# Kernel tuning notes

Measured on AMD Instinct MI355X. Metric: run time of the kernel, lower is better.

## Reference

```python
import jax, jax.numpy as jnp
import numpy as np

# SS2D (VMamba) dims
B, H, W, C = 2, 48, 48, 96
D_INNER, D_STATE, DT_RANK, K = 192, 32, 6, 4


def _silu(x):
    return x * jax.nn.sigmoid(x)


def setup_inputs() -> dict:
    key = jax.random.key(0)
    ks = jax.random.split(key, 8)
    inputs = jax.random.normal(ks[0], (B, H, W, C), jnp.float32)
    in_proj_w = jax.random.normal(ks[1], (2 * D_INNER, C), jnp.float32) * 0.02
    conv_w = jax.random.normal(ks[2], (D_INNER, 1, 3, 3), jnp.float32) * 0.1
    conv_b = jnp.zeros((D_INNER,), jnp.float32)
    x_proj_w = jax.random.normal(ks[3], (K, DT_RANK + 2 * D_STATE, D_INNER), jnp.float32) * 0.02
    dt_projs_w = jax.random.normal(ks[4], (K, D_INNER, DT_RANK), jnp.float32) * 0.1
    dt_projs_b = jax.random.uniform(ks[5], (K, D_INNER), jnp.float32, -4.0, -2.0)
    # S4D-real init: A_log[n] = log(n+1), tiled over K*d_inner
    A_logs = jnp.log(jnp.tile(jnp.arange(1, D_STATE + 1, dtype=jnp.float32), (K * D_INNER, 1)))
    Ds = jnp.ones((K * D_INNER,), jnp.float32)
    ln_w = jnp.ones((D_INNER,), jnp.float32)
    ln_b = jnp.zeros((D_INNER,), jnp.float32)
    out_proj_w = jax.random.normal(ks[6], (C, D_INNER), jnp.float32) * 0.02
    return dict(inputs=inputs, in_proj_w=in_proj_w, conv_w=conv_w, conv_b=conv_b,
                x_proj_w=x_proj_w, dt_projs_w=dt_projs_w, dt_projs_b=dt_projs_b,
                A_logs=A_logs, Ds=Ds, ln_w=ln_w, ln_b=ln_b, out_proj_w=out_proj_w)


def _selective_scan(us, deltas, A, Bs, Cs, Ds_kd):
    # us, deltas: (B,K,d,L); Bs, Cs: (B,K,N,L); A: (K,d,N); Ds_kd: (K,d)
    u_l = jnp.moveaxis(us, -1, 0)      # (L,B,K,d)
    d_l = jnp.moveaxis(deltas, -1, 0)  # (L,B,K,d)
    B_l = jnp.moveaxis(Bs, -1, 0)      # (L,B,K,N)
    C_l = jnp.moveaxis(Cs, -1, 0)      # (L,B,K,N)
    h0 = jnp.zeros(us.shape[:3] + (A.shape[-1],), us.dtype)  # (B,K,d,N)

    def step(h, inp):
        u, d, b, c = inp
        dA = jnp.exp(d[..., None] * A)                    # (B,K,d,N)
        h = h * dA + (d * u)[..., None] * b[:, :, None, :]
        y = jnp.einsum('bkdn,bkn->bkd', h, c)
        return h, y

    _, ys = jax.lax.scan(step, h0, (u_l, d_l, B_l, C_l))
    ys = jnp.moveaxis(ys, 0, -1)  # (B,K,d,L)
    return ys + Ds_kd[None, :, :, None] * us


def _ss2d(x, in_proj_w, conv_w, conv_b, x_proj_w, dt_projs_w, dt_projs_b,
          A_logs, Ds, ln_w, ln_b, out_proj_w):
    b, h, w, c = x.shape
    L = h * w
    xz = jnp.einsum('bhwc,ec->bhwe', x, in_proj_w)          # (B,H,W,2*d_inner)
    x_, z = jnp.split(xz, 2, axis=-1)
    # depthwise 3x3 conv (NCHW), SAME padding
    x_ = jnp.transpose(x_, (0, 3, 1, 2))                    # (B,d,H,W)
    x_ = jax.lax.conv_general_dilated(x_, conv_w, (1, 1), 'SAME',
                                      feature_group_count=D_INNER,
                                      dimension_numbers=('NCHW', 'OIHW', 'NCHW'))
    x_ = _silu(x_ + conv_b[None, :, None, None])
    # 4-direction scan inputs
    x_hw = x_.reshape(b, D_INNER, L)
    x_wh = jnp.transpose(x_, (0, 1, 3, 2)).reshape(b, D_INNER, L)
    xs = jnp.stack([x_hw, x_wh], axis=1)                    # (B,2,d,L)
    xs = jnp.concatenate([xs, jnp.flip(xs, axis=-1)], axis=1)  # (B,4,d,L)
    x_dbl = jnp.einsum('bkdl,kcd->bkcl', xs, x_proj_w)      # (B,4,dt_rank+2N,L)
    dts = x_dbl[:, :, :DT_RANK]
    Bs = x_dbl[:, :, DT_RANK:DT_RANK + D_STATE]
    Cs = x_dbl[:, :, DT_RANK + D_STATE:]
    dts = jnp.einsum('bkrl,kdr->bkdl', dts, dt_projs_w)
    deltas = jax.nn.softplus(dts + dt_projs_b[None, :, :, None])
    A = -jnp.exp(A_logs).reshape(K, D_INNER, D_STATE)
    Ds_kd = Ds.reshape(K, D_INNER)
    out_y = _selective_scan(xs, deltas, A, Bs, Cs, Ds_kd)   # (B,4,d,L)
    inv_y = jnp.flip(out_y[:, 2:4], axis=-1)                # (B,2,d,L)
    wh_y = jnp.transpose(out_y[:, 1].reshape(b, D_INNER, w, h), (0, 1, 3, 2)).reshape(b, D_INNER, L)
    invwh_y = jnp.transpose(inv_y[:, 1].reshape(b, D_INNER, w, h), (0, 1, 3, 2)).reshape(b, D_INNER, L)
    y = out_y[:, 0] + inv_y[:, 0] + wh_y + invwh_y          # (B,d,L)
    y = jnp.transpose(y, (0, 2, 1)).reshape(b, h, w, D_INNER)
    # LayerNorm over channel dim
    mu = jnp.mean(y, axis=-1, keepdims=True)
    var = jnp.var(y, axis=-1, keepdims=True)
    y = (y - mu) * jax.lax.rsqrt(var + 1e-5) * ln_w + ln_b
    y = y * _silu(z)
    return jnp.einsum('bhwd,cd->bhwc', y, out_proj_w)


def reference(inputs, in_proj_w, conv_w, conv_b, x_proj_w, dt_projs_w, dt_projs_b,
              A_logs, Ds, ln_w, ln_b, out_proj_w):
    attn = _ss2d(inputs, in_proj_w, conv_w, conv_b, x_proj_w, dt_projs_w,
                 dt_projs_b, A_logs, Ds, ln_w, ln_b, out_proj_w)
    return inputs + attn
```

## Files before the change

### kernel.cpp

```cpp
#include <hip/hip_runtime.h>
#include <math.h>

#define B_ 2
#define H_ 48
#define W_ 48
#define C_ 96
#define D_ 192
#define L_ 2304
#define K_ 4
#define NS 32
#define RK 6
#define CD 70

#define NC 16
#define CL (L_/NC)
#define NCH (B_*K_*D_)

#define BDL (B_*D_*L_)
#define OFF_Z      0
#define OFF_XPRE   (OFF_Z    + BDL)
#define OFF_XHW    (OFF_XPRE + BDL)
#define OFF_XWH    (OFF_XHW  + BDL)
#define OFF_DELTA  (OFF_XWH  + BDL)
#define OFF_BS     (OFF_DELTA+ B_*K_*D_*L_)
#define OFF_CS     (OFF_BS   + B_*K_*L_*NS)
#define OFF_YS     (OFF_CS   + B_*K_*L_*NS)
#define OFF_YF     (OFF_YS   + B_*K_*L_*D_)

#define OFF_H0     OFF_YF

__global__ __launch_bounds__(256) void k1_inproj(const float* __restrict__ x,
        const float* __restrict__ w, float* __restrict__ ws) {
    __shared__ __align__(16) float Xs[24*128];
    int blk = blockIdx.x;
    int b = blk / 288;
    int rem = blk % 288;
    int l0 = (rem >> 2) * 32;
    int es = rem & 3;
    int tid = threadIdx.x;
    const float4* xs4 = (const float4*)(x + (size_t)(b*L_ + l0)*C_);
    #pragma unroll
    for (int it = 0; it < 3; ++it) {
        int i4 = it*256 + tid;
        float4 v = xs4[i4];
        int idx4 = i4*4;
        int p = idx4 / 96, c = idx4 % 96;
        *(float4*)&Xs[(c>>2)*128 + p*4] = v;
    }
    __syncthreads();
    int l = tid & 31, eg = tid >> 5;
    int pos = l0 + l;
    float acc[12];
    #pragma unroll
    for (int i = 0; i < 12; ++i) acc[i] = 0.f;
    const float4* wp[12];
    #pragma unroll
    for (int i = 0; i < 12; ++i) {
        int e = es*96 + eg*12 + i;
        wp[i] = (const float4*)(w + (size_t)e*96);
    }
    for (int q = 0; q < 24; ++q) {
        float4 xr = *(const float4*)&Xs[q*128 + l*4];
        #pragma unroll
        for (int i = 0; i < 12; ++i) {
            float4 wv = wp[i][q];
            acc[i] += xr.x*wv.x + xr.y*wv.y + xr.z*wv.z + xr.w*wv.w;
        }
    }
    if (es < 2) {
        float* xpre = ws + OFF_XPRE;
        #pragma unroll
        for (int i = 0; i < 12; ++i) {
            int e = es*96 + eg*12 + i;
            xpre[(size_t)(b*D_ + e)*L_ + pos] = acc[i];
        }
    } else {
        float* zp = ws + OFF_Z + (size_t)(b*L_ + pos)*D_ + (es-2)*96 + eg*12;
        #pragma unroll
        for (int q = 0; q < 3; ++q)
            *(float4*)&zp[q*4] = make_float4(acc[q*4], acc[q*4+1], acc[q*4+2], acc[q*4+3]);
    }
}

__global__ __launch_bounds__(256) void k2_conv(const float* __restrict__ cw,
        const float* __restrict__ cb, float* __restrict__ ws) {
    __shared__ float img[26*48];
    __shared__ float res[24*49];
    int blk = blockIdx.x;
    int bd = blk >> 1;
    int half = blk & 1;
    int d = bd % D_;
    int hh0 = half * 24;
    int tid = threadIdx.x;
    const float* xp = ws + OFF_XPRE + (size_t)bd*L_;
    for (int it = 0; it < 5; ++it) {
        int idx = it*256 + tid;
        if (idx < 26*48) {
            int gr = hh0 - 1 + idx/48;
            img[idx] = (gr >= 0 && gr < H_) ? xp[gr*48 + idx%48] : 0.f;
        }
    }
    float wr[9];
    #pragma unroll
    for (int j = 0; j < 9; ++j) wr[j] = cw[d*9 + j];
    float bias = cb[d];
    __syncthreads();
    float* hw = ws + OFF_XHW + (size_t)bd*L_ + hh0*48;
    for (int it = 0; it < 5; ++it) {
        int idx = it*256 + tid;
        if (idx < 24*48) {
            int r = idx/48, w0 = idx%48;
            float acc = bias;
            #pragma unroll
            for (int kh = 0; kh < 3; ++kh) {
                #pragma unroll
                for (int kw = 0; kw < 3; ++kw) {
                    int iw = w0 + kw - 1;
                    if (iw >= 0 && iw < W_)
                        acc = fmaf(img[(r+kh)*48 + iw], wr[kh*3 + kw], acc);
                }
            }
            float v = acc / (1.f + __expf(-acc));
            hw[idx] = v;
            res[r*49 + w0] = v;
        }
    }
    __syncthreads();
    float* wh = ws + OFF_XWH + (size_t)bd*L_;
    for (int it = 0; it < 5; ++it) {
        int idx = it*256 + tid;
        if (idx < 24*48) {
            int w0 = idx/24, r = idx%24;
            wh[w0*48 + hh0 + r] = res[r*49 + w0];
        }
    }
}

__global__ __launch_bounds__(256) void k3_xproj(const float* __restrict__ xpw,
        const float* __restrict__ dtw, const float* __restrict__ dtb,
        float* __restrict__ ws) {
    __shared__ __align__(16) float Xs[48*64];
    __shared__ float xd[CD*17];
    int blk = blockIdx.x;
    int b = blk / 576;
    int rem = blk % 576;
    int k = rem / 144;
    int l0 = (rem % 144) * 16;
    int tid = threadIdx.x;
    const float* src = ws + ((k & 1) ? OFF_XWH : OFF_XHW);
    bool flip = (k >= 2);
    #pragma unroll
    for (int it = 0; it < 12; ++it) {
        int idx = it*256 + tid;
        int d = idx >> 4, l = idx & 15;
        int pos = flip ? (L_ - 1 - (l0 + l)) : (l0 + l);
        Xs[(d>>2)*64 + l*4 + (d&3)] = src[(size_t)(b*D_ + d)*L_ + pos];
    }
    __syncthreads();
    int l = tid & 15, cg = tid >> 4;
    {
        float acc[5] = {0.f, 0.f, 0.f, 0.f, 0.f};
        const float4* wp[5];
        #pragma unroll
        for (int i = 0; i < 5; ++i) {
            int c = cg + 16*i;
            if (c >= CD) c = 0;
            wp[i] = (const float4*)(xpw + ((size_t)k*CD + c)*D_);
        }
        for (int q = 0; q < 48; ++q) {
            float4 xr = *(const float4*)&Xs[q*64 + l*4];
            #pragma unroll
            for (int i = 0; i < 5; ++i) {
                float4 wv = wp[i][q];
                acc[i] += xr.x*wv.x + xr.y*wv.y + xr.z*wv.z + xr.w*wv.w;
            }
        }
        #pragma unroll
        for (int i = 0; i < 5; ++i) {
            int c = cg + 16*i;
            if (c < CD) xd[c*17 + l] = acc[i];
        }
    }
    __syncthreads();
    {
        float r[6];
        #pragma unroll
        for (int rr = 0; rr < 6; ++rr) r[rr] = xd[rr*17 + l];
        float* dout = ws + OFF_DELTA + (size_t)(b*K_ + k)*D_*L_;
        int dg = tid >> 4;
        for (int i = 0; i < 12; ++i) {
            int d = dg*12 + i;
            const float* wdt = dtw + ((size_t)k*D_ + d)*6;
            float acc = dtb[k*D_ + d];
            #pragma unroll
            for (int rr = 0; rr < 6; ++rr) acc = fmaf(r[rr], wdt[rr], acc);
            float sp = fmaxf(acc, 0.f) + log1pf(__expf(-fabsf(acc)));
            dout[(size_t)d*L_ + l0 + l] = sp;
        }
    }
    {
        float* Bsp = ws + OFF_BS + ((size_t)(b*K_ + k)*L_ + l0)*NS;
        float* Csp = ws + OFF_CS + ((size_t)(b*K_ + k)*L_ + l0)*NS;
        int n = tid & 31, lq = tid >> 5;
        #pragma unroll
        for (int j = 0; j < 2; ++j) {
            int ll = lq + 8*j;
            Bsp[(size_t)ll*NS + n] = xd[(RK + n)*17 + ll];
            Csp[(size_t)ll*NS + n] = xd[(RK + NS + n)*17 + ll];
        }
    }
}

__global__ __launch_bounds__(512) void k4a_local(const float* __restrict__ Alogs,
        float* __restrict__ ws) {
    __shared__ float Pl[2][NC][NS];
    __shared__ float Hl[2][NC][NS];
    int blk = blockIdx.x;
    int bk = blk / 96;
    int p = blk % 96;
    int b = bk >> 2, k = bk & 3;
    int c = threadIdx.x >> 5;
    int n = threadIdx.x & 31;
    int dA = 2*p;
    float aA = -__expf(Alogs[((size_t)k*D_ + dA)*NS + n]);
    float aB = -__expf(Alogs[((size_t)k*D_ + dA + 1)*NS + n]);
    const float* dpA = ws + OFF_DELTA + (size_t)(bk*D_ + dA)*L_ + c*CL;
    const float* dpB = dpA + L_;
    const float* uA = ws + ((k & 1) ? OFF_XWH : OFF_XHW) + (size_t)(b*D_ + dA)*L_;
    const float* uB = uA + L_;
    const float* Bsp = ws + OFF_BS + ((size_t)bk*L_ + c*CL)*NS;
    bool flip = (k >= 2);
    float hA = 0.f, hB = 0.f, PA = 1.f, PB = 1.f;
    #pragma unroll 4
    for (int l = 0; l < CL; ++l) {
        int gl = c*CL + l;
        int gu = flip ? (L_ - 1 - gl) : gl;
        float dlA = dpA[l], dlB = dpB[l];
        float uAv = uA[gu], uBv = uB[gu];
        float bn = Bsp[l*NS + n];
        float eA = __expf(dlA * aA);
        float eB = __expf(dlB * aB);
        hA = fmaf(hA, eA, dlA*uAv*bn);
        hB = fmaf(hB, eB, dlB*uBv*bn);
        PA *= eA;
        PB *= eB;
    }
    Pl[0][c][n] = PA; Pl[1][c][n] = PB;
    Hl[0][c][n] = hA; Hl[1][c][n] = hB;
    __syncthreads();
    if (threadIdx.x < 64) {
        int ch = threadIdx.x >> 5, nn = threadIdx.x & 31;
        float* H0p = ws + OFF_H0 + (size_t)(bk*D_ + dA + ch)*NC*NS + nn;
        float h = 0.f;
        #pragma unroll
        for (int cc = 0; cc < NC; ++cc) {
            H0p[cc*NS] = h;
            h = fmaf(h, Pl[ch][cc][nn], Hl[ch][cc][nn]);
        }
    }
}

__global__ __launch_bounds__(512) void k4c_scan(const float* __restrict__ Alogs,
        const float* __restrict__ Dsp, float* __restrict__ ws) {
    __shared__ float yld[CL*32];
    int blk = blockIdx.x;
    int dg = blk % 6;
    int c  = (blk / 6) % NC;
    int bk = blk / (6*NC);
    int b = bk >> 2, k = bk & 3;
    int sw = threadIdx.x >> 5;
    int n  = threadIdx.x & 31;
    int dA = dg*32 + sw;
    int dB = dA + 16;
    float aA = -__expf(Alogs[((size_t)k*D_ + dA)*NS + n]);
    float aB = -__expf(Alogs[((size_t)k*D_ + dB)*NS + n]);
    float dcA = Dsp[k*D_ + dA];
    float dcB = Dsp[k*D_ + dB];
    const float* dpA = ws + OFF_DELTA + (size_t)(bk*D_ + dA)*L_ + c*CL;
    const float* dpB = dpA + 16*L_;
    const float* uA = ws + ((k & 1) ? OFF_XWH : OFF_XHW) + (size_t)(b*D_ + dA)*L_;
    const float* uB = uA + 16*L_;
    const float* Bsp = ws + OFF_BS + ((size_t)bk*L_ + c*CL)*NS;
    const float* Csp = ws + OFF_CS + ((size_t)bk*L_ + c*CL)*NS;
    bool flip = (k >= 2);
    float hA = ws[OFF_H0 + (size_t)(bk*D_ + dA)*NC*NS + c*NS + n];
    float hB = ws[OFF_H0 + (size_t)(bk*D_ + dB)*NC*NS + c*NS + n];
    int g = n >> 3;
    int off = ((g & 1) << 1) | (g >> 1);
    for (int lb = 0; lb < CL; lb += 4) {
        float yA[4], yB[4], uuA[4], uuB[4];
        #pragma unroll
        for (int j = 0; j < 4; ++j) {
            int l = lb + j;
            int gl = c*CL + l;
            int gu = flip ? (L_ - 1 - gl) : gl;
            float dlA = dpA[l], dlB = dpB[l];
            float uAv = uA[gu], uBv = uB[gu];
            float bn = Bsp[l*NS + n];
            float cn = Csp[l*NS + n];
            hA = fmaf(hA, __expf(dlA*aA), dlA*uAv*bn);
            hB = fmaf(hB, __expf(dlB*aB), dlB*uBv*bn);
            yA[j] = hA * cn; yB[j] = hB * cn;
            uuA[j] = uAv;    uuB[j] = uBv;
        }
        #pragma unroll
        for (int j = 0; j < 4; ++j) {
            yA[j] += __shfl_xor(yA[j], 16);
            yB[j] += __shfl_xor(yB[j], 16);
        }
        float zA0 = (n & 16) ? yA[1] : yA[0];
        float zA1 = (n & 16) ? yA[3] : yA[2];
        float zB0 = (n & 16) ? yB[1] : yB[0];
        float zB1 = (n & 16) ? yB[3] : yB[2];
        zA0 += __shfl_xor(zA0, 8); zA1 += __shfl_xor(zA1, 8);
        zB0 += __shfl_xor(zB0, 8); zB1 += __shfl_xor(zB1, 8);
        float wA = (n & 8) ? zA1 : zA0;
        float wB = (n & 8) ? zB1 : zB0;
        wA += __shfl_xor(wA, 4); wA += __shfl_xor(wA, 2); wA += __shfl_xor(wA, 1);
        wB += __shfl_xor(wB, 4); wB += __shfl_xor(wB, 2); wB += __shfl_xor(wB, 1);
        float uaA = (n & 16) ? uuA[1] : uuA[0];
        float ubA = (n & 16) ? uuA[3] : uuA[2];
        float usA = (n & 8) ? ubA : uaA;
        float uaB = (n & 16) ? uuB[1] : uuB[0];
        float ubB = (n & 16) ? uuB[3] : uuB[2];
        float usB = (n & 8) ? ubB : uaB;
        if ((n & 7) == 0) {
            yld[(lb + off)*32 + sw]      = fmaf(dcA, usA, wA);
            yld[(lb + off)*32 + sw + 16] = fmaf(dcB, usB, wB);
        }
    }
    __syncthreads();
    float* ysp = ws + OFF_YS + ((size_t)bk*L_ + c*CL)*D_ + dg*32;
    #pragma unroll
    for (int it = 0; it < 9; ++it) {
        int idx = it*512 + threadIdx.x;
        int l = idx >> 5, dd = idx & 31;
        ysp[(size_t)l*D_ + dd] = yld[idx];
    }
}

__global__ __launch_bounds__(192) void k5_combine(const float* __restrict__ lnw,
        const float* __restrict__ lnb, float* __restrict__ ws) {
    int bp = blockIdx.x;
    int b = bp / L_, pos = bp % L_;
    int d = threadIdx.x;
    int hh = pos / W_, w0 = pos % W_;
    int poswh = w0*H_ + hh;
    const float* ys = ws + OFF_YS + (size_t)b*K_*L_*D_;
    float y = ys[(size_t)(0*L_ + pos)*D_ + d]
            + ys[(size_t)(2*L_ + (L_ - 1 - pos))*D_ + d]
            + ys[(size_t)(1*L_ + poswh)*D_ + d]
            + ys[(size_t)(3*L_ + (L_ - 1 - poswh))*D_ + d];
    float s = y, ss = y*y;
    #pragma unroll
    for (int m = 32; m >= 1; m >>= 1) {
        s  += __shfl_xor(s, m);
        ss += __shfl_xor(ss, m);
    }
    __shared__ float red[2][4];
    int wv = threadIdx.x >> 6;
    if ((threadIdx.x & 63) == 0) { red[0][wv] = s; red[1][wv] = ss; }
    __syncthreads();
    float su = red[0][0] + red[0][1] + red[0][2];
    float sq = red[1][0] + red[1][1] + red[1][2];
    float mu  = su * (1.f/192.f);
    float var = sq * (1.f/192.f) - mu*mu;
    float rs  = rsqrtf(var + 1e-5f);
    float yn = (y - mu)*rs*lnw[d] + lnb[d];
    float zv = ws[OFF_Z + (size_t)(b*L_ + pos)*D_ + d];
    float sz = zv / (1.f + __expf(-zv));
    ws[OFF_YF + (size_t)(b*L_ + pos)*D_ + d] = yn * sz;
}

__global__ __launch_bounds__(256) void k6_outproj(const float* __restrict__ w,
        const float* __restrict__ xin, float* __restrict__ out,
        const float* __restrict__ ws) {
    __shared__ __align__(16) float Ys[48*64];
    __shared__ float outT[16*49];
    int blk = blockIdx.x;
    int b = blk / 288;
    int rem = blk % 288;
    int l0 = (rem >> 1) * 16;
    int es = rem & 1;
    int tid = threadIdx.x;
    const float4* yf4 = (const float4*)(ws + OFF_YF + (size_t)(b*L_ + l0)*D_);
    #pragma unroll
    for (int it = 0; it < 3; ++it) {
        int i4 = it*256 + tid;
        float4 v = yf4[i4];
        int idx4 = i4*4;
        int p = idx4 / 192, dd = idx4 % 192;
        *(float4*)&Ys[(dd>>2)*64 + p*4] = v;
    }
    __syncthreads();
    int l = tid & 15, cg = tid >> 4;
    float acc[3] = {0.f, 0.f, 0.f};
    const float4* wp[3];
    #pragma unroll
    for (int i = 0; i < 3; ++i) {
        int c = es*48 + cg*3 + i;
        wp[i] = (const float4*)(w + (size_t)c*D_);
    }
    for (int q = 0; q < 48; ++q) {
        float4 xr = *(const float4*)&Ys[q*64 + l*4];
        #pragma unroll
        for (int i = 0; i < 3; ++i) {
            float4 wv = wp[i][q];
            acc[i] += xr.x*wv.x + xr.y*wv.y + xr.z*wv.z + xr.w*wv.w;
        }
    }
    #pragma unroll
    for (int i = 0; i < 3; ++i) outT[l*49 + cg*3 + i] = acc[i];
    __syncthreads();
    #pragma unroll
    for (int it = 0; it < 3; ++it) {
        int idx = it*256 + tid;
        int p = idx / 48, cc = idx % 48;
        size_t o = (size_t)(b*L_ + l0 + p)*C_ + es*48 + cc;
        out[o] = xin[o] + outT[p*49 + cc];
    }
}

extern "C" void kernel_launch(void* const* d_in, const int* in_sizes, int n_in,
                              void* d_out, int out_size, void* d_ws, size_t ws_size,
                              hipStream_t stream) {
    const float* x        = (const float*)d_in[0];
    const float* in_proj  = (const float*)d_in[1];
    const float* conv_w   = (const float*)d_in[2];
    const float* conv_b   = (const float*)d_in[3];
    const float* x_proj_w = (const float*)d_in[4];
    const float* dt_w     = (const float*)d_in[5];
    const float* dt_b     = (const float*)d_in[6];
    const float* A_logs   = (const float*)d_in[7];
    const float* Ds       = (const float*)d_in[8];
    const float* ln_w     = (const float*)d_in[9];
    const float* ln_b     = (const float*)d_in[10];
    const float* out_w    = (const float*)d_in[11];
    float* out = (float*)d_out;
    float* ws  = (float*)d_ws;

    k1_inproj <<<576,  256, 0, stream>>>(x, in_proj, ws);
    k2_conv   <<<768,  256, 0, stream>>>(conv_w, conv_b, ws);
    k3_xproj  <<<1152, 256, 0, stream>>>(x_proj_w, dt_w, dt_b, ws);
    k4a_local <<<768,  512, 0, stream>>>(A_logs, ws);
    k4c_scan  <<<768,  512, 0, stream>>>(A_logs, Ds, ws);
    k5_combine<<<B_*L_,192, 0, stream>>>(ln_w, ln_b, ws);
    k6_outproj<<<576,  256, 0, stream>>>(out_w, x, out, ws);
}
```

Before: 284.2 us.

## Transpose B/C layout, vectorize scan loads, use exp2, fuse LayerNorm with out-projection

Stores B and C as (N, L) instead of (L, N) so the scan kernels can read them with float4 loads along L. The chunk-local and chunk scans now load delta, u, B and C as float4, use a native exp2 with prescaled A, and derive the chunk decay product from the sum of deltas. The chunk scan processes 8 steps per iteration, folds the D*u skip term into the reduction, and pads its shared buffer to cut bank conflicts. The combine+LayerNorm+gate kernel is fused with the out-projection, which removes the YF round trip through global memory and one launch. The trade-off is fewer blocks in the fused kernel (288) and higher register pressure in the scan.

Measured after the change: 340.3 us. 19.8% more time.

```diff
diff --git a/kernel.cpp b/kernel.cpp
--- a/kernel.cpp
+++ b/kernel.cpp
@@ -15,6 +15,15 @@
 #define NC 16
 #define CL (L_/NC)
 #define NCH (B_*K_*D_)
+#define LOG2E 1.44269504088896f
+
+__device__ __forceinline__ float fexp2(float x) {
+#if __has_builtin(__builtin_amdgcn_exp2f)
+    return __builtin_amdgcn_exp2f(x);
+#else
+    return __expf(x * 0.69314718055994531f);
+#endif
+}
 
 #define BDL (B_*D_*L_)
 #define OFF_Z      0
@@ -199,14 +208,14 @@
         }
     }
     {
-        float* Bsp = ws + OFF_BS + ((size_t)(b*K_ + k)*L_ + l0)*NS;
-        float* Csp = ws + OFF_CS + ((size_t)(b*K_ + k)*L_ + l0)*NS;
-        int n = tid & 31, lq = tid >> 5;
+        float* Bb = ws + OFF_BS + (size_t)(b*K_ + k)*NS*L_;
+        float* Cb = ws + OFF_CS + (size_t)(b*K_ + k)*NS*L_;
+        int ll = tid & 15, nh = tid >> 4;
         #pragma unroll
         for (int j = 0; j < 2; ++j) {
-            int ll = lq + 8*j;
-            Bsp[(size_t)ll*NS + n] = xd[(RK + n)*17 + ll];
-            Csp[(size_t)ll*NS + n] = xd[(RK + NS + n)*17 + ll];
+            int n = nh + 16*j;
+            Bb[(size_t)n*L_ + l0 + ll] = xd[(RK + n)*17 + ll];
+            Cb[(size_t)n*L_ + l0 + ll] = xd[(RK + NS + n)*17 + ll];
         }
     }
 }
@@ -222,47 +231,67 @@
     int c = threadIdx.x >> 5;
     int n = threadIdx.x & 31;
     int dA = 2*p;
-    float aA = -__expf(Alogs[((size_t)k*D_ + dA)*NS + n]);
-    float aB = -__expf(Alogs[((size_t)k*D_ + dA + 1)*NS + n]);
+    float a2A = -__expf(Alogs[((size_t)k*D_ + dA)*NS + n]) * LOG2E;
+    float a2B = -__expf(Alogs[((size_t)k*D_ + dA + 1)*NS + n]) * LOG2E;
     const float* dpA = ws + OFF_DELTA + (size_t)(bk*D_ + dA)*L_ + c*CL;
     const float* dpB = dpA + L_;
-    const float* uA = ws + ((k & 1) ? OFF_XWH : OFF_XHW) + (size_t)(b*D_ + dA)*L_;
-    const float* uB = uA + L_;
-    const float* Bsp = ws + OFF_BS + ((size_t)bk*L_ + c*CL)*NS;
+    const float* uAp = ws + ((k & 1) ? OFF_XWH : OFF_XHW) + (size_t)(b*D_ + dA)*L_;
+    const float* uBp = uAp + L_;
+    const float* Bp = ws + OFF_BS + ((size_t)bk*NS + n)*L_ + c*CL;
     bool flip = (k >= 2);
-    float hA = 0.f, hB = 0.f, PA = 1.f, PB = 1.f;
-    #pragma unroll 4
-    for (int l = 0; l < CL; ++l) {
-        int gl = c*CL + l;
-        int gu = flip ? (L_ - 1 - gl) : gl;
-        float dlA = dpA[l], dlB = dpB[l];
-        float uAv = uA[gu], uBv = uB[gu];
-        float bn = Bsp[l*NS + n];
-        float eA = __expf(dlA * aA);
-        float eB = __expf(dlB * aB);
-        hA = fmaf(hA, eA, dlA*uAv*bn);
-        hB = fmaf(hB, eB, dlB*uBv*bn);
-        PA *= eA;
-        PB *= eB;
-    }
-    Pl[0][c][n] = PA; Pl[1][c][n] = PB;
+    float hA = 0.f, hB = 0.f, sdA = 0.f, sdB = 0.f;
+    for (int lb = 0; lb < CL; lb += 4) {
+        float4 dA4 = *(const float4*)(dpA + lb);
+        float4 dB4 = *(const float4*)(dpB + lb);
+        float4 b4  = *(const float4*)(Bp + lb);
+        float4 tA4, tB4;
+        if (!flip) {
+            tA4 = *(const float4*)(uAp + c*CL + lb);
+            tB4 = *(const float4*)(uBp + c*CL + lb);
+        } else {
+            float4 rA = *(const float4*)(uAp + (L_ - 4) - (c*CL + lb));
+            float4 rB = *(const float4*)(uBp + (L_ - 4) - (c*CL + lb));
+            tA4 = make_float4(rA.w, rA.z, rA.y, rA.x);
+            tB4 = make_float4(rB.w, rB.z, rB.y, rB.x);
+        }
+        float dlA[4] = {dA4.x, dA4.y, dA4.z, dA4.w};
+        float dlB[4] = {dB4.x, dB4.y, dB4.z, dB4.w};
+        float uuA[4] = {tA4.x, tA4.y, tA4.z, tA4.w};
+        float uuB[4] = {tB4.x, tB4.y, tB4.z, tB4.w};
+        float bb[4]  = {b4.x, b4.y, b4.z, b4.w};
+        #pragma unroll
+        for (int j = 0; j < 4; ++j) {
+            float eA = fexp2(dlA[j]*a2A);
+            float eB = fexp2(dlB[j]*a2B);
+            hA = fmaf(hA, eA, dlA[j]*uuA[j]*bb[j]);
+            hB = fmaf(hB, eB, dlB[j]*uuB[j]*bb[j]);
+            sdA += dlA[j]; sdB += dlB[j];
+        }
+    }
+    Pl[0][c][n] = fexp2(a2A*sdA);
+    Pl[1][c][n] = fexp2(a2B*sdB);
     Hl[0][c][n] = hA; Hl[1][c][n] = hB;
     __syncthreads();
     if (threadIdx.x < 64) {
         int ch = threadIdx.x >> 5, nn = threadIdx.x & 31;
-        float* H0p = ws + OFF_H0 + (size_t)(bk*D_ + dA + ch)*NC*NS + nn;
-        float h = 0.f;
+        float hh = 0.f;
         #pragma unroll
         for (int cc = 0; cc < NC; ++cc) {
-            H0p[cc*NS] = h;
-            h = fmaf(h, Pl[ch][cc][nn], Hl[ch][cc][nn]);
-        }
-    }
+            float pr = Pl[ch][cc][nn];
+            float hf = Hl[ch][cc][nn];
+            Pl[ch][cc][nn] = hh;
+            hh = fmaf(hh, pr, hf);
+        }
+    }
+    __syncthreads();
+    #pragma unroll
+    for (int ch = 0; ch < 2; ++ch)
+        ws[OFF_H0 + (size_t)(bk*D_ + dA + ch)*NC*NS + c*NS + n] = Pl[ch][c][n];
 }
 
 __global__ __launch_bounds__(512) void k4c_scan(const float* __restrict__ Alogs,
         const float* __restrict__ Dsp, float* __restrict__ ws) {
-    __shared__ float yld[CL*32];
+    __shared__ float yld[CL*33];
     int blk = blockIdx.x;
     int dg = blk % 6;
     int c  = (blk / 6) % NC;
@@ -272,61 +301,99 @@
     int n  = threadIdx.x & 31;
     int dA = dg*32 + sw;
     int dB = dA + 16;
-    float aA = -__expf(Alogs[((size_t)k*D_ + dA)*NS + n]);
-    float aB = -__expf(Alogs[((size_t)k*D_ + dB)*NS + n]);
-    float dcA = Dsp[k*D_ + dA];
-    float dcB = Dsp[k*D_ + dB];
+    float a2A = -__expf(Alogs[((size_t)k*D_ + dA)*NS + n]) * LOG2E;
+    float a2B = -__expf(Alogs[((size_t)k*D_ + dB)*NS + n]) * LOG2E;
+    float dc32A = Dsp[k*D_ + dA] * (1.f/32.f);
+    float dc32B = Dsp[k*D_ + dB] * (1.f/32.f);
     const float* dpA = ws + OFF_DELTA + (size_t)(bk*D_ + dA)*L_ + c*CL;
     const float* dpB = dpA + 16*L_;
-    const float* uA = ws + ((k & 1) ? OFF_XWH : OFF_XHW) + (size_t)(b*D_ + dA)*L_;
-    const float* uB = uA + 16*L_;
-    const float* Bsp = ws + OFF_BS + ((size_t)bk*L_ + c*CL)*NS;
-    const float* Csp = ws + OFF_CS + ((size_t)bk*L_ + c*CL)*NS;
+    const float* uAp = ws + ((k & 1) ? OFF_XWH : OFF_XHW) + (size_t)(b*D_ + dA)*L_;
+    const float* uBp = uAp + 16*L_;
+    const float* Bp = ws + OFF_BS + ((size_t)bk*NS + n)*L_ + c*CL;
+    const float* Cp = ws + OFF_CS + ((size_t)bk*NS + n)*L_ + c*CL;
     bool flip = (k >= 2);
     float hA = ws[OFF_H0 + (size_t)(bk*D_ + dA)*NC*NS + c*NS + n];
     float hB = ws[OFF_H0 + (size_t)(bk*D_ + dB)*NC*NS + c*NS + n];
-    int g = n >> 3;
-    int off = ((g & 1) << 1) | (g >> 1);
-    for (int lb = 0; lb < CL; lb += 4) {
-        float yA[4], yB[4], uuA[4], uuB[4];
-        #pragma unroll
-        for (int j = 0; j < 4; ++j) {
-            int l = lb + j;
-            int gl = c*CL + l;
-            int gu = flip ? (L_ - 1 - gl) : gl;
-            float dlA = dpA[l], dlB = dpB[l];
-            float uAv = uA[gu], uBv = uB[gu];
-            float bn = Bsp[l*NS + n];
-            float cn = Csp[l*NS + n];
-            hA = fmaf(hA, __expf(dlA*aA), dlA*uAv*bn);
-            hB = fmaf(hB, __expf(dlB*aB), dlB*uBv*bn);
-            yA[j] = hA * cn; yB[j] = hB * cn;
-            uuA[j] = uAv;    uuB[j] = uBv;
-        }
-        #pragma unroll
-        for (int j = 0; j < 4; ++j) {
+    int off = ((n>>4)&1)*4 + ((n>>3)&1)*2 + ((n>>2)&1);
+    for (int lb = 0; lb < CL; lb += 8) {
+        float dlA[8], dlB[8], uuA[8], uuB[8], bb[8], cc8[8];
+        {
+            float4 a0 = *(const float4*)(dpA + lb);
+            float4 a1 = *(const float4*)(dpA + lb + 4);
+            float4 b0 = *(const float4*)(dpB + lb);
+            float4 b1 = *(const float4*)(dpB + lb + 4);
+            dlA[0]=a0.x; dlA[1]=a0.y; dlA[2]=a0.z; dlA[3]=a0.w;
+            dlA[4]=a1.x; dlA[5]=a1.y; dlA[6]=a1.z; dlA[7]=a1.w;
+            dlB[0]=b0.x; dlB[1]=b0.y; dlB[2]=b0.z; dlB[3]=b0.w;
+            dlB[4]=b1.x; dlB[5]=b1.y; dlB[6]=b1.z; dlB[7]=b1.w;
+            float4 v0 = *(const float4*)(Bp + lb);
+            float4 v1 = *(const float4*)(Bp + lb + 4);
+            bb[0]=v0.x; bb[1]=v0.y; bb[2]=v0.z; bb[3]=v0.w;
+            bb[4]=v1.x; bb[5]=v1.y; bb[6]=v1.z; bb[7]=v1.w;
+            float4 c0 = *(const float4*)(Cp + lb);
+            float4 c1 = *(const float4*)(Cp + lb + 4);
+            cc8[0]=c0.x; cc8[1]=c0.y; cc8[2]=c0.z; cc8[3]=c0.w;
+            cc8[4]=c1.x; cc8[5]=c1.y; cc8[6]=c1.z; cc8[7]=c1.w;
+            if (!flip) {
+                float4 u0 = *(const float4*)(uAp + c*CL + lb);
+                float4 u1 = *(const float4*)(uAp + c*CL + lb + 4);
+                float4 w0 = *(const float4*)(uBp + c*CL + lb);
+                float4 w1 = *(const float4*)(uBp + c*CL + lb + 4);
+                uuA[0]=u0.x; uuA[1]=u0.y; uuA[2]=u0.z; uuA[3]=u0.w;
+                uuA[4]=u1.x; uuA[5]=u1.y; uuA[6]=u1.z; uuA[7]=u1.w;
+                uuB[0]=w0.x; uuB[1]=w0.y; uuB[2]=w0.z; uuB[3]=w0.w;
+                uuB[4]=w1.x; uuB[5]=w1.y; uuB[6]=w1.z; uuB[7]=w1.w;
+            } else {
+                float4 u0 = *(const float4*)(uAp + (L_ - 4) - (c*CL + lb));
+                float4 u1 = *(const float4*)(uAp + (L_ - 8) - (c*CL + lb));
+                float4 w0 = *(const float4*)(uBp + (L_ - 4) - (c*CL + lb));
+                float4 w1 = *(const float4*)(uBp + (L_ - 8) - (c*CL + lb));
+                uuA[0]=u0.w; uuA[1]=u0.z; uuA[2]=u0.y; uuA[3]=u0.x;
+                uuA[4]=u1.w; uuA[5]=u1.z; uuA[6]=u1.y; uuA[7]=u1.x;
+                uuB[0]=w0.w; uuB[1]=w0.z; uuB[2]=w0.y; uuB[3]=w0.x;
+                uuB[4]=w1.w; uuB[5]=w1.z; uuB[6]=w1.y; uuB[7]=w1.x;
+            }
+        }
+        float yA[8], yB[8];
+        #pragma unroll
+        for (int j = 0; j < 8; ++j) {
+            float eA = fexp2(dlA[j]*a2A);
+            float eB = fexp2(dlB[j]*a2B);
+            hA = fmaf(hA, eA, dlA[j]*uuA[j]*bb[j]);
+            hB = fmaf(hB, eB, dlB[j]*uuB[j]*bb[j]);
+            yA[j] = fmaf(hA, cc8[j], dc32A*uuA[j]);
+            yB[j] = fmaf(hB, cc8[j], dc32B*uuB[j]);
+        }
+        #pragma unroll
+        for (int j = 0; j < 8; ++j) {
             yA[j] += __shfl_xor(yA[j], 16);
             yB[j] += __shfl_xor(yB[j], 16);
         }
-        float zA0 = (n & 16) ? yA[1] : yA[0];
-        float zA1 = (n & 16) ? yA[3] : yA[2];
-        float zB0 = (n & 16) ? yB[1] : yB[0];
-        float zB1 = (n & 16) ? yB[3] : yB[2];
+        float zA0 = (n & 16) ? yA[4] : yA[0];
+        float zA1 = (n & 16) ? yA[5] : yA[1];
+        float zA2 = (n & 16) ? yA[6] : yA[2];
+        float zA3 = (n & 16) ? yA[7] : yA[3];
+        float zB0 = (n & 16) ? yB[4] : yB[0];
+        float zB1 = (n & 16) ? yB[5] : yB[1];
+        float zB2 = (n & 16) ? yB[6] : yB[2];
+        float zB3 = (n & 16) ? yB[7] : yB[3];
         zA0 += __shfl_xor(zA0, 8); zA1 += __shfl_xor(zA1, 8);
+        zA2 += __shfl_xor(zA2, 8); zA3 += __shfl_xor(zA3, 8);
         zB0 += __shfl_xor(zB0, 8); zB1 += __shfl_xor(zB1, 8);
-        float wA = (n & 8) ? zA1 : zA0;
-        float wB = (n & 8) ? zB1 : zB0;
-        wA += __shfl_xor(wA, 4); wA += __shfl_xor(wA, 2); wA += __shfl_xor(wA, 1);
-        wB += __shfl_xor(wB, 4); wB += __shfl_xor(wB, 2); wB += __shfl_xor(wB, 1);
-        float uaA = (n & 16) ? uuA[1] : uuA[0];
-        float ubA = (n & 16) ? uuA[3] : uuA[2];
-        float usA = (n & 8) ? ubA : uaA;
-        float uaB = (n & 16) ? uuB[1] : uuB[0];
-        float ubB = (n & 16) ? uuB[3] : uuB[2];
-        float usB = (n & 8) ? ubB : uaB;
-        if ((n & 7) == 0) {
-            yld[(lb + off)*32 + sw]      = fmaf(dcA, usA, wA);
-            yld[(lb + off)*32 + sw + 16] = fmaf(dcB, usB, wB);
+        zB2 += __shfl_xor(zB2, 8); zB3 += __shfl_xor(zB3, 8);
+        float wA0 = (n & 8) ? zA2 : zA0;
+        float wA1 = (n & 8) ? zA3 : zA1;
+        float wB0 = (n & 8) ? zB2 : zB0;
+        float wB1 = (n & 8) ? zB3 : zB1;
+        wA0 += __shfl_xor(wA0, 4); wA1 += __shfl_xor(wA1, 4);
+        wB0 += __shfl_xor(wB0, 4); wB1 += __shfl_xor(wB1, 4);
+        float tA = (n & 4) ? wA1 : wA0;
+        float tB = (n & 4) ? wB1 : wB0;
+        tA += __shfl_xor(tA, 2); tA += __shfl_xor(tA, 1);
+        tB += __shfl_xor(tB, 2); tB += __shfl_xor(tB, 1);
+        if ((n & 3) == 0) {
+            yld[(lb + off)*33 + sw]      = tA;
+            yld[(lb + off)*33 + sw + 16] = tB;
         }
     }
     __syncthreads();
@@ -335,89 +402,98 @@
     for (int it = 0; it < 9; ++it) {
         int idx = it*512 + threadIdx.x;
         int l = idx >> 5, dd = idx & 31;
-        ysp[(size_t)l*D_ + dd] = yld[idx];
-    }
-}
-
-__global__ __launch_bounds__(192) void k5_combine(const float* __restrict__ lnw,
-        const float* __restrict__ lnb, float* __restrict__ ws) {
-    int bp = blockIdx.x;
-    int b = bp / L_, pos = bp % L_;
-    int d = threadIdx.x;
-    int hh = pos / W_, w0 = pos % W_;
-    int poswh = w0*H_ + hh;
-    const float* ys = ws + OFF_YS + (size_t)b*K_*L_*D_;
-    float y = ys[(size_t)(0*L_ + pos)*D_ + d]
-            + ys[(size_t)(2*L_ + (L_ - 1 - pos))*D_ + d]
-            + ys[(size_t)(1*L_ + poswh)*D_ + d]
-            + ys[(size_t)(3*L_ + (L_ - 1 - poswh))*D_ + d];
-    float s = y, ss = y*y;
-    #pragma unroll
-    for (int m = 32; m >= 1; m >>= 1) {
-        s  += __shfl_xor(s, m);
-        ss += __shfl_xor(ss, m);
-    }
-    __shared__ float red[2][4];
-    int wv = threadIdx.x >> 6;
-    if ((threadIdx.x & 63) == 0) { red[0][wv] = s; red[1][wv] = ss; }
-    __syncthreads();
-    float su = red[0][0] + red[0][1] + red[0][2];
-    float sq = red[1][0] + red[1][1] + red[1][2];
-    float mu  = su * (1.f/192.f);
-    float var = sq * (1.f/192.f) - mu*mu;
-    float rs  = rsqrtf(var + 1e-5f);
-    float yn = (y - mu)*rs*lnw[d] + lnb[d];
-    float zv = ws[OFF_Z + (size_t)(b*L_ + pos)*D_ + d];
-    float sz = zv / (1.f + __expf(-zv));
-    ws[OFF_YF + (size_t)(b*L_ + pos)*D_ + d] = yn * sz;
-}
-
-__global__ __launch_bounds__(256) void k6_outproj(const float* __restrict__ w,
+        ysp[(size_t)l*D_ + dd] = yld[l*33 + dd];
+    }
+}
+
+__global__ __launch_bounds__(256) void k56_fused(const float* __restrict__ lnw,
+        const float* __restrict__ lnb, const float* __restrict__ w,
         const float* __restrict__ xin, float* __restrict__ out,
         const float* __restrict__ ws) {
-    __shared__ __align__(16) float Ys[48*64];
-    __shared__ float outT[16*49];
+    __shared__ __align__(16) float YsT[16*196];
+    __shared__ float psum[16][17], psq[16][17];
+    __shared__ float outT[16*97];
     int blk = blockIdx.x;
-    int b = blk / 288;
-    int rem = blk % 288;
-    int l0 = (rem >> 1) * 16;
-    int es = rem & 1;
+    int b = blk / 144;
+    int l0 = (blk % 144) * 16;
     int tid = threadIdx.x;
-    const float4* yf4 = (const float4*)(ws + OFF_YF + (size_t)(b*L_ + l0)*D_);
-    #pragma unroll
-    for (int it = 0; it < 3; ++it) {
-        int i4 = it*256 + tid;
-        float4 v = yf4[i4];
-        int idx4 = i4*4;
-        int p = idx4 / 192, dd = idx4 % 192;
-        *(float4*)&Ys[(dd>>2)*64 + p*4] = v;
-    }
-    __syncthreads();
-    int l = tid & 15, cg = tid >> 4;
-    float acc[3] = {0.f, 0.f, 0.f};
-    const float4* wp[3];
-    #pragma unroll
-    for (int i = 0; i < 3; ++i) {
-        int c = es*48 + cg*3 + i;
-        wp[i] = (const float4*)(w + (size_t)c*D_);
-    }
-    for (int q = 0; q < 48; ++q) {
-        float4 xr = *(const float4*)&Ys[q*64 + l*4];
-        #pragma unroll
-        for (int i = 0; i < 3; ++i) {
-            float4 wv = wp[i][q];
-            acc[i] += xr.x*wv.x + xr.y*wv.y + xr.z*wv.z + xr.w*wv.w;
-        }
-    }
-    #pragma unroll
-    for (int i = 0; i < 3; ++i) outT[l*49 + cg*3 + i] = acc[i];
-    __syncthreads();
-    #pragma unroll
-    for (int it = 0; it < 3; ++it) {
+    {
+        int p = tid >> 4, dg = tid & 15;
+        int pos = l0 + p;
+        int hh = pos / W_, w0 = pos % W_;
+        int poswh = w0*H_ + hh;
+        const float* ysb = ws + OFF_YS + (size_t)b*K_*L_*D_;
+        const float* r0 = ysb + (size_t)(0*L_ + pos)*D_;
+        const float* r1 = ysb + (size_t)(1*L_ + poswh)*D_;
+        const float* r2 = ysb + (size_t)(2*L_ + (L_-1-pos))*D_;
+        const float* r3 = ysb + (size_t)(3*L_ + (L_-1-poswh))*D_;
+        float yv[12];
+        float s = 0.f, sq = 0.f;
+        #pragma unroll
+        for (int i = 0; i < 12; i += 4) {
+            int d = dg*12 + i;
+            float4 v0 = *(const float4*)(r0 + d);
+            float4 v1 = *(const float4*)(r1 + d);
+            float4 v2 = *(const float4*)(r2 + d);
+            float4 v3 = *(const float4*)(r3 + d);
+            float y0 = v0.x+v1.x+v2.x+v3.x;
+            float y1 = v0.y+v1.y+v2.y+v3.y;
+            float y2 = v0.z+v1.z+v2.z+v3.z;
+            float y3 = v0.w+v1.w+v2.w+v3.w;
+            yv[i]=y0; yv[i+1]=y1; yv[i+2]=y2; yv[i+3]=y3;
+            s += y0+y1+y2+y3;
+            sq += y0*y0+y1*y1+y2*y2+y3*y3;
+        }
+        psum[p][dg] = s; psq[p][dg] = sq;
+        __syncthreads();
+        float su = 0.f, ssq = 0.f;
+        #pragma unroll
+        for (int j = 0; j < 16; ++j) { su += psum[p][j]; ssq += psq[p][j]; }
+        float mu  = su * (1.f/192.f);
+        float var = ssq * (1.f/192.f) - mu*mu;
+        float rs  = rsqrtf(var + 1e-5f);
+        const float* zp = ws + OFF_Z + (size_t)(b*L_ + pos)*D_;
+        #pragma unroll
+        for (int i = 0; i < 12; i += 4) {
+            int d = dg*12 + i;
+            float4 o;
+            float* oo = (float*)&o;
+            #pragma unroll
+            for (int jj = 0; jj < 4; ++jj) {
+                float yn = (yv[i+jj] - mu)*rs*lnw[d+jj] + lnb[d+jj];
+                float zv = zp[d+jj];
+                float sz = zv / (1.f + __expf(-zv));
+                oo[jj] = yn * sz;
+            }
+            *(float4*)&YsT[p*196 + d] = o;
+        }
+    }
+    __syncthreads();
+    {
+        int l = tid & 15, cg = tid >> 4;
+        float acc[6] = {0.f,0.f,0.f,0.f,0.f,0.f};
+        const float4* wp[6];
+        #pragma unroll
+        for (int i = 0; i < 6; ++i)
+            wp[i] = (const float4*)(w + (size_t)(cg*6 + i)*D_);
+        for (int q = 0; q < 48; ++q) {
+            float4 xr = *(const float4*)&YsT[l*196 + q*4];
+            #pragma unroll
+            for (int i = 0; i < 6; ++i) {
+                float4 wv = wp[i][q];
+                acc[i] += xr.x*wv.x + xr.y*wv.y + xr.z*wv.z + xr.w*wv.w;
+            }
+        }
+        #pragma unroll
+        for (int i = 0; i < 6; ++i) outT[l*97 + cg*6 + i] = acc[i];
+    }
+    __syncthreads();
+    #pragma unroll
+    for (int it = 0; it < 6; ++it) {
         int idx = it*256 + tid;
-        int p = idx / 48, cc = idx % 48;
-        size_t o = (size_t)(b*L_ + l0 + p)*C_ + es*48 + cc;
-        out[o] = xin[o] + outT[p*49 + cc];
+        int p = idx / 96, cc = idx % 96;
+        size_t o = (size_t)(b*L_ + l0 + p)*C_ + cc;
+        out[o] = xin[o] + outT[p*97 + cc];
     }
 }
 
@@ -444,6 +520,5 @@
     k3_xproj  <<<1152, 256, 0, stream>>>(x_proj_w, dt_w, dt_b, ws);
     k4a_local <<<768,  512, 0, stream>>>(A_logs, ws);
     k4c_scan  <<<768,  512, 0, stream>>>(A_logs, Ds, ws);
-    k5_combine<<<B_*L_,192, 0, stream>>>(ln_w, ln_b, ws);
-    k6_outproj<<<576,  256, 0, stream>>>(out_w, x, out, ws);
-}
+    k56_fused <<<288,  256, 0, stream>>>(ln_w, ln_b, out_w, x, out, ws);
+}
```
